# Kernel optimization log

Hardware: AMD Instinct MI355X
Metric: run time of the kernel (lower is better)

The kernel has to match this reference:

```python
import jax, jax.numpy as jnp
import numpy as np

NUM_BLOCKS = 4
B, S, D = 4, 4096, 1024
A, FF = 1024, 4096
LN_EPS = 1e-6


def _ln(x, s, b):
    m = jnp.mean(x, axis=-1, keepdims=True)
    v = jnp.mean(jnp.square(x - m), axis=-1, keepdims=True)
    return (x - m) * jax.lax.rsqrt(v + LN_EPS) * s + b


def setup_inputs() -> dict:
    key = jax.random.key(0)
    ks = jax.random.split(key, 8)
    w = lambda k, shape: jax.random.normal(k, shape, dtype=jnp.float32) * 0.02
    return {
        "x": jax.random.normal(ks[0], (B, S, D), dtype=jnp.float32),
        "Wq": w(ks[1], (NUM_BLOCKS, D, A)), "bq": jnp.zeros((NUM_BLOCKS, A), jnp.float32),
        "Wk": w(ks[2], (NUM_BLOCKS, D, A)), "bk": jnp.zeros((NUM_BLOCKS, A), jnp.float32),
        "Wv": w(ks[3], (NUM_BLOCKS, D, A)), "bv": jnp.zeros((NUM_BLOCKS, A), jnp.float32),
        "Wo": w(ks[4], (NUM_BLOCKS, A, D)), "bo": jnp.zeros((NUM_BLOCKS, D), jnp.float32),
        "ln1_s": jnp.ones((NUM_BLOCKS, D), jnp.float32), "ln1_b": jnp.zeros((NUM_BLOCKS, D), jnp.float32),
        "W1": w(ks[5], (NUM_BLOCKS, D, FF)), "b1": jnp.zeros((NUM_BLOCKS, FF), jnp.float32),
        "W2": w(ks[6], (NUM_BLOCKS, FF, D)), "b2": jnp.zeros((NUM_BLOCKS, D), jnp.float32),
        "ln2_s": jnp.ones((NUM_BLOCKS, D), jnp.float32), "ln2_b": jnp.zeros((NUM_BLOCKS, D), jnp.float32),
    }


def reference(x, Wq, bq, Wk, bk, Wv, bv, Wo, bo, ln1_s, ln1_b,
              W1, b1, W2, b2, ln2_s, ln2_b):
    for i in range(NUM_BLOCKS):
        residual = x
        # --- linear attention (elu+1 feature map, elementwise KV aggregation) ---
        q = x @ Wq[i] + bq[i]            # [B,S,A]
        k = x @ Wk[i] + bk[i]
        v = x @ Wv[i] + bv[i]
        Q = jax.nn.elu(q) + 1.0
        K = jax.nn.elu(k) + 1.0
        KV = jnp.einsum('nsh,nsh->nh', K, v, precision='highest')   # [B,A]
        Ksum = jnp.sum(K, axis=1)                                    # [B,A]
        Z = 1.0 / (Q * Ksum[:, None, :] + 1e-6)
        V = Q * KV[:, None, :] * Z                                   # [B,S,A]
        a = jax.nn.gelu(V @ Wo[i] + bo[i])   # gelu inside LinearAttention
        a = jax.nn.gelu(a)                   # gelu in the block body
        x = _ln(a + residual, ln1_s[i], ln1_b[i])
        # --- feedforward ---
        residual = x
        h = jax.nn.gelu(x @ W1[i] + b1[i])
        f = jax.nn.gelu(h @ W2[i] + b2[i])
        x = _ln(f + residual, ln2_s[i], ln2_b[i])
    return x
```

## Files before the change

### kernel.cpp

```cpp
#include <hip/hip_runtime.h>
#include <hip/hip_bf16.h>

typedef unsigned short u16;

#define B_  4
#define S_  4096
#define D_  1024
#define A_  1024
#define FF_ 4096
#define NB  4
#define LN_EPS 1e-6f

typedef __bf16 bf16x8 __attribute__((ext_vector_type(8)));
typedef float  floatx4 __attribute__((ext_vector_type(4)));

__device__ __forceinline__ float gelu_f(float x) {
    float u = 0.7978845608028654f * (x + 0.044715f * x * x * x);
    return x / (1.0f + __expf(-2.0f * u));
}

__device__ __forceinline__ u16 f2bf(float f) {
    __bf16 h = (__bf16)f;
    return *(u16*)&h;
}

__device__ __forceinline__ float bf2f(u16 u) {
    unsigned int v = ((unsigned int)u) << 16;
    float f;
    __builtin_memcpy(&f, &v, 4);
    return f;
}

__device__ __forceinline__ void gload_lds16(const u16* g, u16* l) {
    __builtin_amdgcn_global_load_lds(
        (const __attribute__((address_space(1))) void*)g,
        (__attribute__((address_space(3))) void*)l, 16, 0, 0);
}

__global__ __launch_bounds__(256) void zero_kv(float* __restrict__ p) {
    int idx = (blockIdx.x * 256 + threadIdx.x) * 4;
    *(float4*)(p + idx) = (float4){0.f, 0.f, 0.f, 0.f};
}

__global__ __launch_bounds__(256) void transpose_w(const float* __restrict__ W,
                                                   u16* __restrict__ Wt,
                                                   int K, int N) {
    __shared__ float tile[32][33];
    int tx = threadIdx.x;
    int ty = threadIdx.y;
    int n0 = blockIdx.x * 32;
    int k0 = blockIdx.y * 32;
#pragma unroll
    for (int r = 0; r < 4; r++) {
        int k = k0 + ty + r * 8;
        tile[ty + r * 8][tx] = W[(size_t)k * N + n0 + tx];
    }
    __syncthreads();
#pragma unroll
    for (int r = 0; r < 4; r++) {
        int n = n0 + ty + r * 8;
        Wt[(size_t)n * K + k0 + tx] = f2bf(tile[tx][ty + r * 8]);
    }
}

#define BAR  { asm volatile("" ::: "memory"); __builtin_amdgcn_s_barrier(); \
               asm volatile("" ::: "memory"); }
#define VMC(N) asm volatile("s_waitcnt vmcnt(" #N ")" ::: "memory")
#define PRIO1 __builtin_amdgcn_s_setprio(1)
#define PRIO0 __builtin_amdgcn_s_setprio(0)

#define STG(OFF, P, H, KT) {                                                   \
    const u16* s_ = (P) + (size_t)((H) * 128) * K + (KT) * 64;                 \
    u16* d_ = shm + (OFF) + (H) * 8192 + t * 8;                                \
    gload_lds16(s_, d_);                                                       \
    gload_lds16(s_ + (size_t)64 * K, d_ + 4096); }

#define LDA4(OFF, IH) {                                                        \
    _Pragma("unroll") for (int ii = 0; ii < 4; ii++) {                         \
        const u16* p_ = shm + (OFF) + aro + ((IH) * 4 + ii) * 1024;            \
        a[ii][0] = *(const bf16x8*)(p_ + sl0);                                 \
        a[ii][1] = *(const bf16x8*)(p_ + sl1); } }

#define LDB2(OFF, JH) {                                                        \
    _Pragma("unroll") for (int jj = 0; jj < 2; jj++) {                         \
        const u16* p_ = shm + (OFF) + bro + ((JH) * 2 + jj) * 1024;            \
        b[(JH) * 2 + jj][0] = *(const bf16x8*)(p_ + sl0);                      \
        b[(JH) * 2 + jj][1] = *(const bf16x8*)(p_ + sl1); } }

#define MM(IH, JH) {                                                           \
    _Pragma("unroll") for (int ii = 0; ii < 4; ii++)                           \
    _Pragma("unroll") for (int jj = 0; jj < 2; jj++)                           \
    _Pragma("unroll") for (int s = 0; s < 2; s++)                              \
        acc[(IH) * 4 + ii][(JH) * 2 + jj] =                                    \
            __builtin_amdgcn_mfma_f32_16x16x32_bf16(                           \
                a[ii][s], b[(JH) * 2 + jj][s],                                 \
                acc[(IH) * 4 + ii][(JH) * 2 + jj], 0, 0, 0); }

template <int MODE>
__global__ __launch_bounds__(512, 2) void gemm256(
    const u16* __restrict__ Amat, const u16* __restrict__ Bt,
    const float* __restrict__ bias, u16* __restrict__ out,
    int M, int N, int K, int gx, int ldo,
    u16* __restrict__ outK, u16* __restrict__ outV,
    const float* __restrict__ biasK, const float* __restrict__ biasV)
{
    __shared__ u16 shm[81920];

    const int nwg  = (int)gridDim.x;
    const int cpx  = nwg >> 3;
    const int wgid = ((int)blockIdx.x & 7) * cpx + ((int)blockIdx.x >> 3);
    const int bx = wgid % gx;
    const int by = wgid / gx;
    const int m0 = by * 256, n0 = bx * 256;

    const int t    = threadIdx.x;
    const int wid  = t >> 6, lane = t & 63;
    const int wm   = wid >> 2, wn = wid & 3;
    const int lm   = lane & 15, quad = lane >> 4;

    const int trow  = t >> 3;
    const int tslot = (t & 7) ^ (trow & 7);
    const u16* pa = Amat + (size_t)(m0 + trow) * K + tslot * 8;
    const u16* pb = Bt   + (size_t)(n0 + trow) * K + tslot * 8;

    const int aro = (wm * 128 + lm) * 64;
    const int bro = (wn * 64  + lm) * 64;
    const int sl0 = ((0 * 4 + quad) ^ (lm & 7)) * 8;
    const int sl1 = ((1 * 4 + quad) ^ (lm & 7)) * 8;

    floatx4 acc[8][4];
#pragma unroll
    for (int i = 0; i < 8; i++)
#pragma unroll
        for (int j = 0; j < 4; j++) acc[i][j] = (floatx4){0.f, 0.f, 0.f, 0.f};

    bf16x8 a[4][2], b[4][2];

    const int NT = K >> 6;

    STG(0,     pa, 0, 0); STG(0,     pa, 1, 0);
    STG(32768, pb, 0, 0); STG(32768, pb, 1, 0);
    STG(49152, pb, 0, 1); STG(49152, pb, 1, 1);
    VMC(4); BAR;

    int aCur = 0,     aNxt = 16384;
    int bB0 = 32768,  bB1 = 49152, bB2 = 65536;

    for (int tt = 0; tt < NT; tt++) {
        int t1 = tt + 1; if (t1 > NT - 1) t1 = NT - 1;
        int t2 = tt + 2; if (t2 > NT - 1) t2 = NT - 1;
        LDA4(aCur, 0); LDB2(bB0, 0);
        STG(aNxt, pa, 0, t1);
        BAR; PRIO1; MM(0, 0); PRIO0;
        LDB2(bB0, 1);
        STG(aNxt, pa, 1, t1);
        BAR; PRIO1; MM(0, 1); PRIO0;
        LDA4(aCur, 1);
        STG(bB2, pb, 0, t2);
        BAR; PRIO1; MM(1, 1); PRIO0;
        STG(bB2, pb, 1, t2);
        VMC(4);
        BAR; PRIO1; MM(1, 0); PRIO0;
        int tmp = aCur; aCur = aNxt; aNxt = tmp;
        tmp = bB0; bB0 = bB1; bB1 = bB2; bB2 = tmp;
    }

    asm volatile("s_waitcnt vmcnt(0)" ::: "memory");
    __syncthreads();

    const float* bp; u16* ob; int c0; bool elu;
    if (MODE == 4) {
        int seg = n0 >> 10;
        bp  = (seg == 0) ? bias : (seg == 1) ? biasK : biasV;
        ob  = (seg == 0) ? out  : (seg == 1) ? outK  : outV;
        c0  = n0 & 1023;
        elu = (seg < 2);
    } else { bp = bias; ob = out; c0 = n0; elu = false; }

    u16* Ct = shm;
#pragma unroll
    for (int j = 0; j < 4; j++) {
        int cl   = wn * 64 + j * 16 + lm;
        float bvl = bp[c0 + cl];
#pragma unroll
        for (int i = 0; i < 8; i++) {
            int rl = wm * 128 + i * 16 + quad * 4;
#pragma unroll
            for (int r = 0; r < 4; r++) {
                float z = acc[i][j][r] + bvl;
                float o;
                if (MODE == 2)      o = gelu_f(gelu_f(z));
                else if (MODE == 3) o = gelu_f(z);
                else if (MODE == 4) o = elu ? ((z > 0.f) ? z + 1.f : __expf(z)) : z;
                else                o = z;
                Ct[(rl + r) * 264 + cl] = f2bf(o);
            }
        }
    }
    __syncthreads();

    {
        int row = t >> 1;
        int ch  = (t & 1) * 128;
        const u16* src = Ct + row * 264 + ch;
        u16* dst = ob + (size_t)(m0 + row) * ldo + c0 + ch;
#pragma unroll
        for (int cc = 0; cc < 128; cc += 8)
            *(uint4*)(dst + cc) = *(const uint4*)(src + cc);
    }
}

__global__ __launch_bounds__(256) void kv_reduce(const u16* __restrict__ Kb,
                                                 const u16* __restrict__ vb,
                                                 float* __restrict__ KV,
                                                 float* __restrict__ Ks) {
    int n  = blockIdx.z;
    int h  = threadIdx.x * 4;
    int s0 = blockIdx.y * 128;
    const u16* kp = Kb + (size_t)n * S_ * A_ + (size_t)s0 * A_ + h;
    const u16* vp = vb + (size_t)n * S_ * A_ + (size_t)s0 * A_ + h;
    float kv0 = 0.f, kv1 = 0.f, kv2 = 0.f, kv3 = 0.f;
    float ks0 = 0.f, ks1 = 0.f, ks2 = 0.f, ks3 = 0.f;
#pragma unroll 4
    for (int s = 0; s < 128; s++) {
        ushort4 k4 = *(const ushort4*)(kp + (size_t)s * A_);
        ushort4 v4 = *(const ushort4*)(vp + (size_t)s * A_);
        float k0 = bf2f(k4.x), k1 = bf2f(k4.y), k2 = bf2f(k4.z), k3 = bf2f(k4.w);
        kv0 += k0 * bf2f(v4.x); kv1 += k1 * bf2f(v4.y);
        kv2 += k2 * bf2f(v4.z); kv3 += k3 * bf2f(v4.w);
        ks0 += k0; ks1 += k1; ks2 += k2; ks3 += k3;
    }
    int base = n * A_ + h;
    atomicAdd(&KV[base + 0], kv0); atomicAdd(&KV[base + 1], kv1);
    atomicAdd(&KV[base + 2], kv2); atomicAdd(&KV[base + 3], kv3);
    atomicAdd(&Ks[base + 0], ks0); atomicAdd(&Ks[base + 1], ks1);
    atomicAdd(&Ks[base + 2], ks2); atomicAdd(&Ks[base + 3], ks3);
}

__global__ __launch_bounds__(256) void linattn_ew(const u16* __restrict__ Qb,
                                                  const float* __restrict__ KV,
                                                  const float* __restrict__ Ks,
                                                  u16* __restrict__ vout) {
    size_t idx = ((size_t)blockIdx.x * 256 + threadIdx.x) * 4;
    int n = (int)(idx >> 22);
    int h = (int)(idx & (A_ - 1));
    ushort4 q4 = *(const ushort4*)(Qb + idx);
    int base = n * A_ + h;
    float4 kv4 = *(const float4*)(KV + base);
    float4 ks4 = *(const float4*)(Ks + base);
    float q0 = bf2f(q4.x), q1 = bf2f(q4.y), q2 = bf2f(q4.z), q3 = bf2f(q4.w);
    float o0 = q0 * kv4.x / (q0 * ks4.x + 1e-6f);
    float o1 = q1 * kv4.y / (q1 * ks4.y + 1e-6f);
    float o2 = q2 * kv4.z / (q2 * ks4.z + 1e-6f);
    float o3 = q3 * kv4.w / (q3 * ks4.w + 1e-6f);
    ushort4 o;
    o.x = f2bf(o0); o.y = f2bf(o1); o.z = f2bf(o2); o.w = f2bf(o3);
    *(ushort4*)(vout + idx) = o;
}

__global__ __launch_bounds__(256) void convert_x(const float* __restrict__ x,
                                                 float* __restrict__ xf,
                                                 u16* __restrict__ xb) {
    size_t idx = ((size_t)blockIdx.x * 256 + threadIdx.x) * 4;
    float4 v = *(const float4*)(x + idx);
    *(float4*)(xf + idx) = v;
    ushort4 o;
    o.x = f2bf(v.x); o.y = f2bf(v.y); o.z = f2bf(v.z); o.w = f2bf(v.w);
    *(ushort4*)(xb + idx) = o;
}

__global__ __launch_bounds__(256) void ln_fused(const u16* y,
                                                const float* res,
                                                const float* sc,
                                                const float* bs,
                                                float* xf,
                                                u16* xb) {
    __shared__ float wred[8];
    int row = blockIdx.x;
    int t   = threadIdx.x;
    int lane = t & 63, wid = t >> 6;
    const u16*   yp = y   + (size_t)row * D_;
    const float* rp = res + (size_t)row * D_;
    ushort4 y4 = *(const ushort4*)(yp + t * 4);
    float4  r4 = *(const float4*)(rp + t * 4);
    float v0 = bf2f(y4.x) + r4.x;
    float v1 = bf2f(y4.y) + r4.y;
    float v2 = bf2f(y4.z) + r4.z;
    float v3 = bf2f(y4.w) + r4.w;
    float s = v0 + v1 + v2 + v3;
#pragma unroll
    for (int o = 32; o; o >>= 1) s += __shfl_down(s, o, 64);
    if (lane == 0) wred[wid] = s;
    __syncthreads();
    float mean = (wred[0] + wred[1] + wred[2] + wred[3]) * (1.0f / D_);
    float d0 = v0 - mean, d1 = v1 - mean, d2 = v2 - mean, d3 = v3 - mean;
    float q = d0 * d0 + d1 * d1 + d2 * d2 + d3 * d3;
#pragma unroll
    for (int o = 32; o; o >>= 1) q += __shfl_down(q, o, 64);
    if (lane == 0) wred[wid + 4] = q;
    __syncthreads();
    float rstd = rsqrtf((wred[4] + wred[5] + wred[6] + wred[7]) * (1.0f / D_) + LN_EPS);
    float4 s4 = *(const float4*)(sc + t * 4);
    float4 b4 = *(const float4*)(bs + t * 4);
    float o0 = d0 * rstd * s4.x + b4.x;
    float o1 = d1 * rstd * s4.y + b4.y;
    float o2 = d2 * rstd * s4.z + b4.z;
    float o3 = d3 * rstd * s4.w + b4.w;
    *(float4*)(xf + (size_t)row * D_ + t * 4) = (float4){o0, o1, o2, o3};
    ushort4 ob;
    ob.x = f2bf(o0); ob.y = f2bf(o1); ob.z = f2bf(o2); ob.w = f2bf(o3);
    *(ushort4*)(xb + (size_t)row * D_ + t * 4) = ob;
}

extern "C" void kernel_launch(void* const* d_in, const int* in_sizes, int n_in,
                              void* d_out, int out_size, void* d_ws, size_t ws_size,
                              hipStream_t stream) {
    const float* x_in = (const float*)d_in[0];
    const float* Wq   = (const float*)d_in[1];
    const float* bq   = (const float*)d_in[2];
    const float* Wk   = (const float*)d_in[3];
    const float* bk   = (const float*)d_in[4];
    const float* Wv   = (const float*)d_in[5];
    const float* bv   = (const float*)d_in[6];
    const float* Wo   = (const float*)d_in[7];
    const float* bo   = (const float*)d_in[8];
    const float* ln1s = (const float*)d_in[9];
    const float* ln1b = (const float*)d_in[10];
    const float* W1   = (const float*)d_in[11];
    const float* b1   = (const float*)d_in[12];
    const float* W2   = (const float*)d_in[13];
    const float* b2   = (const float*)d_in[14];
    const float* ln2s = (const float*)d_in[15];
    const float* ln2b = (const float*)d_in[16];

    const size_t MB = 1024 * 1024;
    char* ws = (char*)d_ws;
    float* xf    = (float*)d_out;
    u16*   xb    = (u16*)(ws);
    u16*   Qb    = (u16*)(ws + 32 * MB);
    u16*   Kb    = (u16*)(ws + 64 * MB);
    u16*   vb    = (u16*)(ws + 96 * MB);
    u16*   hid   = (u16*)(ws + 32 * MB);
    u16*   WtQKV = (u16*)(ws + 128 * MB);
    u16*   Wot   = (u16*)(ws + 134 * MB);
    float* kvb   = (float*)(ws + 136 * MB);
    u16*   W1t   = (u16*)(ws + 160 * MB);
    u16*   W2t   = (u16*)(ws + 168 * MB);
    float* KV    = kvb;
    float* Ks    = kvb + B_ * A_;

    const int M = B_ * S_;

    convert_x<<<dim3(M * D_ / 1024), 256, 0, stream>>>(x_in, xf, xb);

    for (int i = 0; i < NB; i++) {
        const float* Wq_i = Wq + (size_t)i * D_ * A_;
        const float* Wk_i = Wk + (size_t)i * D_ * A_;
        const float* Wv_i = Wv + (size_t)i * D_ * A_;
        const float* Wo_i = Wo + (size_t)i * A_ * D_;
        const float* W1_i = W1 + (size_t)i * D_ * FF_;
        const float* W2_i = W2 + (size_t)i * FF_ * D_;

        transpose_w<<<dim3(A_ / 32, D_ / 32), dim3(32, 8), 0, stream>>>(Wq_i, WtQKV, D_, A_);
        transpose_w<<<dim3(A_ / 32, D_ / 32), dim3(32, 8), 0, stream>>>(Wk_i, WtQKV + (size_t)A_ * D_, D_, A_);
        transpose_w<<<dim3(A_ / 32, D_ / 32), dim3(32, 8), 0, stream>>>(Wv_i, WtQKV + (size_t)2 * A_ * D_, D_, A_);
        transpose_w<<<dim3(D_ / 32, A_ / 32), dim3(32, 8), 0, stream>>>(Wo_i, Wot, A_, D_);
        transpose_w<<<dim3(FF_ / 32, D_ / 32), dim3(32, 8), 0, stream>>>(W1_i, W1t, D_, FF_);
        transpose_w<<<dim3(D_ / 32, FF_ / 32), dim3(32, 8), 0, stream>>>(W2_i, W2t, FF_, D_);

        gemm256<4><<<dim3(12 * 64), 512, 0, stream>>>(
            xb, WtQKV, bq + i * A_, Qb, M, 3072, D_, 12, 1024,
            Kb, vb, bk + i * A_, bv + i * A_);

        zero_kv<<<dim3(8), 256, 0, stream>>>(kvb);
        kv_reduce<<<dim3(1, S_ / 128, B_), 256, 0, stream>>>(Kb, vb, KV, Ks);

        linattn_ew<<<dim3(M * A_ / 1024), 256, 0, stream>>>(Qb, KV, Ks, Kb);

        gemm256<2><<<dim3(4 * 64), 512, 0, stream>>>(
            Kb, Wot, bo + i * D_, vb, M, D_, A_, 4, 1024,
            nullptr, nullptr, nullptr, nullptr);

        ln_fused<<<dim3(M), 256, 0, stream>>>(vb, xf, ln1s + i * D_, ln1b + i * D_, xf, xb);

        gemm256<3><<<dim3(16 * 64), 512, 0, stream>>>(
            xb, W1t, b1 + (size_t)i * FF_, hid, M, FF_, D_, 16, 4096,
            nullptr, nullptr, nullptr, nullptr);
        gemm256<3><<<dim3(4 * 64), 512, 0, stream>>>(
            hid, W2t, b2 + i * D_, xb, M, D_, FF_, 4, 1024,
            nullptr, nullptr, nullptr, nullptr);

        ln_fused<<<dim3(M), 256, 0, stream>>>(xb, xf, ln2s + i * D_, ln2b + i * D_, xf, xb);
    }
}
```

Baseline: 2.682 ms.

## Replace 256x256 eight-wave GEMM with simpler 128x128 four-wave double-buffered GEMM

```diff
diff --git a/kernel.cpp b/kernel.cpp
--- a/kernel.cpp
+++ b/kernel.cpp
@@ -69,68 +69,50 @@
 #define PRIO1 __builtin_amdgcn_s_setprio(1)
 #define PRIO0 __builtin_amdgcn_s_setprio(0)
 
-#define STG(OFF, P, H, KT) {                                                   \
-    const u16* s_ = (P) + (size_t)((H) * 128) * K + (KT) * 64;                 \
-    u16* d_ = shm + (OFF) + (H) * 8192 + t * 8;                                \
-    gload_lds16(s_, d_);                                                       \
-    gload_lds16(s_ + (size_t)64 * K, d_ + 4096); }
-
-#define LDA4(OFF, IH) {                                                        \
-    _Pragma("unroll") for (int ii = 0; ii < 4; ii++) {                         \
-        const u16* p_ = shm + (OFF) + aro + ((IH) * 4 + ii) * 1024;            \
-        a[ii][0] = *(const bf16x8*)(p_ + sl0);                                 \
-        a[ii][1] = *(const bf16x8*)(p_ + sl1); } }
-
-#define LDB2(OFF, JH) {                                                        \
-    _Pragma("unroll") for (int jj = 0; jj < 2; jj++) {                         \
-        const u16* p_ = shm + (OFF) + bro + ((JH) * 2 + jj) * 1024;            \
-        b[(JH) * 2 + jj][0] = *(const bf16x8*)(p_ + sl0);                      \
-        b[(JH) * 2 + jj][1] = *(const bf16x8*)(p_ + sl1); } }
-
-#define MM(IH, JH) {                                                           \
-    _Pragma("unroll") for (int ii = 0; ii < 4; ii++)                           \
-    _Pragma("unroll") for (int jj = 0; jj < 2; jj++)                           \
-    _Pragma("unroll") for (int s = 0; s < 2; s++)                              \
-        acc[(IH) * 4 + ii][(JH) * 2 + jj] =                                    \
-            __builtin_amdgcn_mfma_f32_16x16x32_bf16(                           \
-                a[ii][s], b[(JH) * 2 + jj][s],                                 \
-                acc[(IH) * 4 + ii][(JH) * 2 + jj], 0, 0, 0); }
+#define STG(OFF, P, KT) {                                                      \
+    const u16* s_ = (P) + (size_t)(KT) * 64;                                   \
+    u16* d_ = shm + (OFF) + d0;                                                \
+    gload_lds16(s_,                 d_);                                       \
+    gload_lds16(s_ + (size_t)8 * K,  d_ + 512);                                \
+    gload_lds16(s_ + (size_t)16 * K, d_ + 1024);                               \
+    gload_lds16(s_ + (size_t)24 * K, d_ + 1536); }
 
 template <int MODE>
-__global__ __launch_bounds__(512, 2) void gemm256(
+__global__ __launch_bounds__(256, 2) void gemm128(
     const u16* __restrict__ Amat, const u16* __restrict__ Bt,
     const float* __restrict__ bias, u16* __restrict__ out,
     int M, int N, int K, int gx, int ldo,
     u16* __restrict__ outK, u16* __restrict__ outV,
     const float* __restrict__ biasK, const float* __restrict__ biasV)
 {
-    __shared__ u16 shm[81920];
+    __shared__ u16 shm[32768];
 
     const int nwg  = (int)gridDim.x;
     const int cpx  = nwg >> 3;
     const int wgid = ((int)blockIdx.x & 7) * cpx + ((int)blockIdx.x >> 3);
     const int bx = wgid % gx;
     const int by = wgid / gx;
-    const int m0 = by * 256, n0 = bx * 256;
+    const int m0 = by * 128, n0 = bx * 128;
 
     const int t    = threadIdx.x;
     const int wid  = t >> 6, lane = t & 63;
-    const int wm   = wid >> 2, wn = wid & 3;
+    const int wm   = wid >> 1, wn = wid & 1;
     const int lm   = lane & 15, quad = lane >> 4;
 
-    const int trow  = t >> 3;
-    const int tslot = (t & 7) ^ (trow & 7);
-    const u16* pa = Amat + (size_t)(m0 + trow) * K + tslot * 8;
-    const u16* pb = Bt   + (size_t)(n0 + trow) * K + tslot * 8;
-
-    const int aro = (wm * 128 + lm) * 64;
-    const int bro = (wn * 64  + lm) * 64;
+    const int trow0 = (t >> 6) * 32 + ((t >> 3) & 7);
+    const int tslot = (t & 7) ^ ((t >> 3) & 7);
+    const int d0    = (t >> 6) * 2048 + (t & 63) * 8;
+    const u16* pa = Amat + (size_t)(m0 + trow0) * K + tslot * 8;
+    const u16* pb = Bt   + (size_t)(n0 + trow0) * K + tslot * 8;
+
+    const int aro = (wm * 64 + lm) * 64;
+    const int bro = (wn * 64 + lm) * 64;
     const int sl0 = ((0 * 4 + quad) ^ (lm & 7)) * 8;
     const int sl1 = ((1 * 4 + quad) ^ (lm & 7)) * 8;
 
-    floatx4 acc[8][4];
-#pragma unroll
-    for (int i = 0; i < 8; i++)
+    floatx4 acc[4][4];
+#pragma unroll
+    for (int i = 0; i < 4; i++)
 #pragma unroll
         for (int j = 0; j < 4; j++) acc[i][j] = (floatx4){0.f, 0.f, 0.f, 0.f};
 
@@ -138,35 +120,42 @@
 
     const int NT = K >> 6;
 
-    STG(0,     pa, 0, 0); STG(0,     pa, 1, 0);
-    STG(32768, pb, 0, 0); STG(32768, pb, 1, 0);
-    STG(49152, pb, 0, 1); STG(49152, pb, 1, 1);
-    VMC(4); BAR;
-
-    int aCur = 0,     aNxt = 16384;
-    int bB0 = 32768,  bB1 = 49152, bB2 = 65536;
-
+    STG(0,    pa, 0);
+    STG(8192, pb, 0);
+    VMC(0); BAR;
+
+    int cur = 0;
     for (int tt = 0; tt < NT; tt++) {
-        int t1 = tt + 1; if (t1 > NT - 1) t1 = NT - 1;
-        int t2 = tt + 2; if (t2 > NT - 1) t2 = NT - 1;
-        LDA4(aCur, 0); LDB2(bB0, 0);
-        STG(aNxt, pa, 0, t1);
-        BAR; PRIO1; MM(0, 0); PRIO0;
-        LDB2(bB0, 1);
-        STG(aNxt, pa, 1, t1);
-        BAR; PRIO1; MM(0, 1); PRIO0;
-        LDA4(aCur, 1);
-        STG(bB2, pb, 0, t2);
-        BAR; PRIO1; MM(1, 1); PRIO0;
-        STG(bB2, pb, 1, t2);
-        VMC(4);
-        BAR; PRIO1; MM(1, 0); PRIO0;
-        int tmp = aCur; aCur = aNxt; aNxt = tmp;
-        tmp = bB0; bB0 = bB1; bB1 = bB2; bB2 = tmp;
-    }
-
-    asm volatile("s_waitcnt vmcnt(0)" ::: "memory");
-    __syncthreads();
+        int tn = tt + 1; if (tn > NT - 1) tn = NT - 1;
+        int nxt = 16384 - cur;
+        STG(nxt,        pa, tn);
+        STG(nxt + 8192, pb, tn);
+#pragma unroll
+        for (int i = 0; i < 4; i++) {
+            const u16* p_ = shm + cur + aro + i * 1024;
+            a[i][0] = *(const bf16x8*)(p_ + sl0);
+            a[i][1] = *(const bf16x8*)(p_ + sl1);
+        }
+#pragma unroll
+        for (int j = 0; j < 4; j++) {
+            const u16* p_ = shm + cur + 8192 + bro + j * 1024;
+            b[j][0] = *(const bf16x8*)(p_ + sl0);
+            b[j][1] = *(const bf16x8*)(p_ + sl1);
+        }
+        PRIO1;
+#pragma unroll
+        for (int i = 0; i < 4; i++)
+#pragma unroll
+            for (int j = 0; j < 4; j++)
+#pragma unroll
+                for (int s = 0; s < 2; s++)
+                    acc[i][j] = __builtin_amdgcn_mfma_f32_16x16x32_bf16(
+                        a[i][s], b[j][s], acc[i][j], 0, 0, 0);
+        PRIO0;
+        VMC(0);
+        BAR;
+        cur = nxt;
+    }
 
     const float* bp; u16* ob; int c0; bool elu;
     if (MODE == 4) {
@@ -183,8 +172,8 @@
         int cl   = wn * 64 + j * 16 + lm;
         float bvl = bp[c0 + cl];
 #pragma unroll
-        for (int i = 0; i < 8; i++) {
-            int rl = wm * 128 + i * 16 + quad * 4;
+        for (int i = 0; i < 4; i++) {
+            int rl = wm * 64 + i * 16 + quad * 4;
 #pragma unroll
             for (int r = 0; r < 4; r++) {
                 float z = acc[i][j][r] + bvl;
@@ -193,7 +182,7 @@
                 else if (MODE == 3) o = gelu_f(z);
                 else if (MODE == 4) o = elu ? ((z > 0.f) ? z + 1.f : __expf(z)) : z;
                 else                o = z;
-                Ct[(rl + r) * 264 + cl] = f2bf(o);
+                Ct[(rl + r) * 136 + cl] = f2bf(o);
             }
         }
     }
@@ -201,11 +190,11 @@
 
     {
         int row = t >> 1;
-        int ch  = (t & 1) * 128;
-        const u16* src = Ct + row * 264 + ch;
+        int ch  = (t & 1) * 64;
+        const u16* src = Ct + row * 136 + ch;
         u16* dst = ob + (size_t)(m0 + row) * ldo + c0 + ch;
 #pragma unroll
-        for (int cc = 0; cc < 128; cc += 8)
+        for (int cc = 0; cc < 64; cc += 8)
             *(uint4*)(dst + cc) = *(const uint4*)(src + cc);
     }
 }
@@ -368,8 +357,8 @@
         transpose_w<<<dim3(FF_ / 32, D_ / 32), dim3(32, 8), 0, stream>>>(W1_i, W1t, D_, FF_);
         transpose_w<<<dim3(D_ / 32, FF_ / 32), dim3(32, 8), 0, stream>>>(W2_i, W2t, FF_, D_);
 
-        gemm256<4><<<dim3(12 * 64), 512, 0, stream>>>(
-            xb, WtQKV, bq + i * A_, Qb, M, 3072, D_, 12, 1024,
+        gemm128<4><<<dim3(24 * 128), 256, 0, stream>>>(
+            xb, WtQKV, bq + i * A_, Qb, M, 3072, D_, 24, 1024,
             Kb, vb, bk + i * A_, bv + i * A_);
 
         zero_kv<<<dim3(8), 256, 0, stream>>>(kvb);
@@ -377,17 +366,17 @@
 
         linattn_ew<<<dim3(M * A_ / 1024), 256, 0, stream>>>(Qb, KV, Ks, Kb);
 
-        gemm256<2><<<dim3(4 * 64), 512, 0, stream>>>(
-            Kb, Wot, bo + i * D_, vb, M, D_, A_, 4, 1024,
+        gemm128<2><<<dim3(8 * 128), 256, 0, stream>>>(
+            Kb, Wot, bo + i * D_, vb, M, D_, A_, 8, 1024,
             nullptr, nullptr, nullptr, nullptr);
 
         ln_fused<<<dim3(M), 256, 0, stream>>>(vb, xf, ln1s + i * D_, ln1b + i * D_, xf, xb);
 
-        gemm256<3><<<dim3(16 * 64), 512, 0, stream>>>(
-            xb, W1t, b1 + (size_t)i * FF_, hid, M, FF_, D_, 16, 4096,
+        gemm128<3><<<dim3(32 * 128), 256, 0, stream>>>(
+            xb, W1t, b1 + (size_t)i * FF_, hid, M, FF_, D_, 32, 4096,
             nullptr, nullptr, nullptr, nullptr);
-        gemm256<3><<<dim3(4 * 64), 512, 0, stream>>>(
-            hid, W2t, b2 + i * D_, xb, M, D_, FF_, 4, 1024,
+        gemm128<3><<<dim3(8 * 128), 256, 0, stream>>>(
+            hid, W2t, b2 + i * D_, xb, M, D_, FF_, 8, 1024,
             nullptr, nullptr, nullptr, nullptr);
 
         ln_fused<<<dim3(M), 256, 0, stream>>>(xb, xf, ln2s + i * D_, ln2b + i * D_, xf, xb);
```

Result: slower. 2.816 ms (+5.0%).
